# Kernel tuning notes

Hardware: AMD Instinct MI355X
Metric: run time of the kernel (lower is better)

Reference implementation:

```python
import jax, jax.numpy as jnp
import numpy as np

N = 50000
E = 800000
NFEAT, NHID, NCLASS = 128, 128, 40


def setup_inputs() -> dict:
    key = jax.random.key(0)
    ks = jax.random.split(key, 8)
    x = jax.random.normal(ks[0], (N, NFEAT), dtype=jnp.float32)
    edge_index = jax.random.randint(ks[1], (2, E), 0, N, dtype=jnp.int64)
    def glorot(k, fan_in, fan_out):
        s = jnp.sqrt(6.0 / (fan_in + fan_out)).astype(jnp.float32)
        return jax.random.uniform(k, (fan_in, fan_out), jnp.float32, -s, s)
    W1 = glorot(ks[2], NFEAT, NHID); b1 = jnp.zeros((NHID,), jnp.float32)
    W2 = glorot(ks[3], NHID, NHID);  b2 = jnp.zeros((NHID,), jnp.float32)
    W3 = glorot(ks[4], NHID, NCLASS); b3 = jnp.zeros((NCLASS,), jnp.float32)
    return {"x": x, "edge_index": edge_index,
            "W1": W1, "b1": b1, "W2": W2, "b2": b2, "W3": W3, "b3": b3}


def _gcn_norm(edge_index, num_nodes, dtype):
    # Add self-loops, then symmetric normalization D^-1/2 (A+I) D^-1/2 (PyG gcn_norm).
    loop = jnp.arange(num_nodes, dtype=edge_index.dtype)
    src = jnp.concatenate([edge_index[0], loop])
    dst = jnp.concatenate([edge_index[1], loop])
    deg = jax.ops.segment_sum(jnp.ones_like(src, dtype=dtype), dst, num_segments=num_nodes)
    dinv = jnp.where(deg > 0, deg ** -0.5, 0.0).astype(dtype)
    norm = dinv[src] * dinv[dst]  # [E+N]
    return src, dst, norm


def _gcn_conv(h, src, dst, norm, W, b, num_nodes):
    h = h @ W                              # dense transform first (out_dim small)
    msg = h[src] * norm[:, None]           # gather + per-edge scale
    out = jax.ops.segment_sum(msg, dst, num_segments=num_nodes)  # scatter-add
    return out + b


def reference(x, edge_index, W1, b1, W2, b2, W3, b3):
    src, dst, norm = _gcn_norm(edge_index, N, x.dtype)
    h = jax.nn.relu(_gcn_conv(x, src, dst, norm, W1, b1, N))  # dropout: eval mode (identity)
    h = jax.nn.relu(_gcn_conv(h, src, dst, norm, W2, b2, N))
    h = _gcn_conv(h, src, dst, norm, W3, b3, N)
    return jax.nn.log_softmax(h, axis=-1)
```

## Files before the change

### kernel.cpp

```cpp
#include <hip/hip_runtime.h>
#include <stdint.h>

#define NN 50000
#define NE 800000
#define GG 782
#define NB 196
#define EB 3125

typedef __attribute__((ext_vector_type(8))) short bfx8;
typedef __attribute__((ext_vector_type(4))) float f32x4;

__device__ inline unsigned short f2bf(float f) {
    union { float f; uint32_t u; } x; x.f = f;
    uint32_t u = x.u;
    return (unsigned short)((u + 0x7fffu + ((u >> 16) & 1u)) >> 16);
}
__device__ inline uint32_t pack2bf(float lo, float hi) {
    return (uint32_t)f2bf(lo) | ((uint32_t)f2bf(hi) << 16);
}
__device__ inline float bf2f(unsigned short h) {
    union { uint32_t u; float f; } c; c.u = ((uint32_t)h) << 16;
    return c.f;
}
__device__ inline float2 bfp2f2(uint32_t v) {
    union { uint32_t u; float f; } a, b;
    a.u = (v & 0xffffu) << 16;
    b.u = v & 0xffff0000u;
    return make_float2(a.f, b.f);
}
__device__ inline bfx8 ld8(const unsigned short* p) {
    union { uint4 u; bfx8 v; } c;
    c.u = *(const uint4*)p;
    return c.v;
}
__device__ inline bfx8 cvt8(float4 u, float4 v) {
    union { unsigned short s[8]; bfx8 r; } c;
    c.s[0] = f2bf(u.x); c.s[1] = f2bf(u.y); c.s[2] = f2bf(u.z); c.s[3] = f2bf(u.w);
    c.s[4] = f2bf(v.x); c.s[5] = f2bf(v.y); c.s[6] = f2bf(v.z); c.s[7] = f2bf(v.w);
    return c.r;
}

__global__ void prep(const float* __restrict__ W1, const float* __restrict__ W2,
                     const float* __restrict__ W3,
                     unsigned short* __restrict__ WT1, unsigned short* __restrict__ WT2,
                     unsigned short* __restrict__ WT3, int* __restrict__ hist) {
    int bid = blockIdx.x;
    if (bid < 152) {
        int w = bid * 256 + threadIdx.x;
        if (w < 16384) {
            int nn = w >> 7, k = w & 127;
            WT1[nn * 128 + k] = f2bf(W1[k * 128 + nn]);
        } else if (w < 32768) {
            int w2 = w - 16384, nn = w2 >> 7, k = w2 & 127;
            WT2[nn * 128 + k] = f2bf(W2[k * 128 + nn]);
        } else if (w < 38912) {
            int w2 = w - 32768, nn = w2 >> 7, k = w2 & 127;
            WT3[nn * 128 + k] = (nn < 40) ? f2bf(W3[k * 40 + nn]) : (unsigned short)0;
        }
    } else {
        int i = (bid - 152) * 256 + threadIdx.x;
        if (i < NN) hist[i] = 0;
    }
}

__global__ __launch_bounds__(256) void gemm1_hist(const float* __restrict__ X,
                                                  const unsigned short* __restrict__ WT,
                                                  unsigned short* __restrict__ G, int n,
                                                  const int* __restrict__ dst,
                                                  int* __restrict__ hist,
                                                  unsigned short* __restrict__ rank, int e) {
    if (blockIdx.x >= GG) {
        int i = (blockIdx.x - GG) * 256 + threadIdx.x;
        if (i < e) rank[i] = (unsigned short)atomicAdd(hist + dst[i], 1);
        return;
    }
    int wave = threadIdx.x >> 6;
    int lane = threadIdx.x & 63;
    int quad = lane >> 4;
    int c = lane & 15;
    int rowbase = blockIdx.x * 64 + wave * 16;

    int arow = rowbase + c;
    if (arow >= n) arow = n - 1;
    const float* ap = X + (size_t)arow * 128 + quad * 8;
    bfx8 a[4];
#pragma unroll
    for (int kc = 0; kc < 4; kc++) {
        float4 u = *(const float4*)(ap + kc * 32);
        float4 v = *(const float4*)(ap + kc * 32 + 4);
        a[kc] = cvt8(u, v);
    }

    f32x4 acc[8];
#pragma unroll
    for (int ct = 0; ct < 8; ct++) acc[ct] = (f32x4){0.f, 0.f, 0.f, 0.f};
#pragma unroll
    for (int ct = 0; ct < 8; ct++) {
        const unsigned short* bp = WT + (size_t)(ct * 16 + c) * 128 + quad * 8;
#pragma unroll
        for (int kc = 0; kc < 4; kc++) {
            bfx8 b = ld8(bp + kc * 32);
            acc[ct] = __builtin_amdgcn_mfma_f32_16x16x32_bf16(a[kc], b, acc[ct], 0, 0, 0);
        }
    }

    int r0 = rowbase + quad * 4;
    bool odd = lane & 1;
#pragma unroll
    for (int ct = 0; ct < 8; ct++) {
        float x0 = acc[ct][0], x1 = acc[ct][1], x2 = acc[ct][2], x3 = acc[ct][3];
        float y0 = __shfl_xor(x0, 1, 64), y1 = __shfl_xor(x1, 1, 64);
        float y2 = __shfl_xor(x2, 1, 64), y3 = __shfl_xor(x3, 1, 64);
        int colp = ct * 16 + (c & ~1);
        if (!odd) {
            if (r0 + 0 < n) *(uint32_t*)(&G[(size_t)(r0 + 0) * 128 + colp]) = pack2bf(x0, y0);
            if (r0 + 1 < n) *(uint32_t*)(&G[(size_t)(r0 + 1) * 128 + colp]) = pack2bf(x1, y1);
        } else {
            if (r0 + 2 < n) *(uint32_t*)(&G[(size_t)(r0 + 2) * 128 + colp]) = pack2bf(y2, x2);
            if (r0 + 3 < n) *(uint32_t*)(&G[(size_t)(r0 + 3) * 128 + colp]) = pack2bf(y3, x3);
        }
    }
}

__global__ void scan_dinv(const int* __restrict__ hist, int* row_ptr, int* bsum,
                          float* dinv, int n) {
    __shared__ int s[256];
    int tid = threadIdx.x;
    int i = blockIdx.x * 256 + tid;
    int v = (i < n) ? hist[i] : 0;
    s[tid] = v;
    __syncthreads();
#pragma unroll
    for (int off = 1; off < 256; off <<= 1) {
        int y = (tid >= off) ? s[tid - off] : 0;
        __syncthreads();
        s[tid] += y;
        __syncthreads();
    }
    if (i < n) {
        row_ptr[i] = s[tid] - v;
        dinv[i] = rsqrtf(1.0f + (float)v);
    }
    if (tid == 255) bsum[blockIdx.x] = s[255];
}

__global__ void bucket_k(const int* __restrict__ src, const int* __restrict__ dst,
                         const int* __restrict__ row_ptr, const int* __restrict__ bsum,
                         const unsigned short* __restrict__ rank,
                         unsigned short* __restrict__ csr_src, int* __restrict__ boff_g,
                         int e) {
    __shared__ int s[256];
    __shared__ int bex[256];
    int tid = threadIdx.x;
    int v = (tid < NB) ? bsum[tid] : 0;
    s[tid] = v;
    __syncthreads();
#pragma unroll
    for (int off = 1; off < 256; off <<= 1) {
        int y = (tid >= off) ? s[tid - off] : 0;
        __syncthreads();
        s[tid] += y;
        __syncthreads();
    }
    bex[tid] = s[tid] - v;
    __syncthreads();

    if (blockIdx.x == gridDim.x - 1) {
        if (tid < NB) boff_g[tid] = bex[tid];
        return;
    }
    int i = blockIdx.x * 256 + tid;
    if (i < e) {
        int d = dst[i];
        csr_src[row_ptr[d] + bex[d >> 8] + (int)rank[i]] = (unsigned short)src[i];
    }
}

__global__ __launch_bounds__(256) void gemm128_mfma(const unsigned short* __restrict__ A,
                                                    const unsigned short* __restrict__ WT,
                                                    const float* __restrict__ dinv,
                                                    unsigned short* __restrict__ G, int n) {
    int wave = threadIdx.x >> 6;
    int lane = threadIdx.x & 63;
    int quad = lane >> 4;
    int c = lane & 15;
    int rowbase = blockIdx.x * 64 + wave * 16;

    int arow = rowbase + c;
    if (arow >= n) arow = n - 1;
    const unsigned short* ap = A + (size_t)arow * 128 + quad * 8;
    bfx8 a[4];
#pragma unroll
    for (int kc = 0; kc < 4; kc++) a[kc] = ld8(ap + kc * 32);

    f32x4 acc[8];
#pragma unroll
    for (int ct = 0; ct < 8; ct++) acc[ct] = (f32x4){0.f, 0.f, 0.f, 0.f};
#pragma unroll
    for (int ct = 0; ct < 8; ct++) {
        const unsigned short* bp = WT + (size_t)(ct * 16 + c) * 128 + quad * 8;
#pragma unroll
        for (int kc = 0; kc < 4; kc++) {
            bfx8 b = ld8(bp + kc * 32);
            acc[ct] = __builtin_amdgcn_mfma_f32_16x16x32_bf16(a[kc], b, acc[ct], 0, 0, 0);
        }
    }

    int r0 = rowbase + quad * 4;
    float di[4];
#pragma unroll
    for (int r = 0; r < 4; r++) {
        int rr = r0 + r;
        di[r] = dinv[rr < n ? rr : 0];
    }
    bool odd = lane & 1;
#pragma unroll
    for (int ct = 0; ct < 8; ct++) {
        float x0 = acc[ct][0], x1 = acc[ct][1], x2 = acc[ct][2], x3 = acc[ct][3];
        float y0 = __shfl_xor(x0, 1, 64), y1 = __shfl_xor(x1, 1, 64);
        float y2 = __shfl_xor(x2, 1, 64), y3 = __shfl_xor(x3, 1, 64);
        int colp = ct * 16 + (c & ~1);
        if (!odd) {
            if (r0 + 0 < n) *(uint32_t*)(&G[(size_t)(r0 + 0) * 128 + colp]) = pack2bf(di[0] * x0, di[0] * y0);
            if (r0 + 1 < n) *(uint32_t*)(&G[(size_t)(r0 + 1) * 128 + colp]) = pack2bf(di[1] * x1, di[1] * y1);
        } else {
            if (r0 + 2 < n) *(uint32_t*)(&G[(size_t)(r0 + 2) * 128 + colp]) = pack2bf(di[2] * y2, di[2] * x2);
            if (r0 + 3 < n) *(uint32_t*)(&G[(size_t)(r0 + 3) * 128 + colp]) = pack2bf(di[3] * y3, di[3] * x3);
        }
    }
}

__global__ __launch_bounds__(256) void gemm40_mfma(const unsigned short* __restrict__ A,
                                                   const unsigned short* __restrict__ WT,
                                                   const float* __restrict__ dinv,
                                                   unsigned short* __restrict__ G, int n) {
    int wave = threadIdx.x >> 6;
    int lane = threadIdx.x & 63;
    int quad = lane >> 4;
    int c = lane & 15;
    int rowbase = blockIdx.x * 64 + wave * 16;

    int arow = rowbase + c;
    if (arow >= n) arow = n - 1;
    const unsigned short* ap = A + (size_t)arow * 128 + quad * 8;
    bfx8 a[4];
#pragma unroll
    for (int kc = 0; kc < 4; kc++) a[kc] = ld8(ap + kc * 32);

    f32x4 acc[3];
#pragma unroll
    for (int ct = 0; ct < 3; ct++) acc[ct] = (f32x4){0.f, 0.f, 0.f, 0.f};
#pragma unroll
    for (int ct = 0; ct < 3; ct++) {
        const unsigned short* bp = WT + (size_t)(ct * 16 + c) * 128 + quad * 8;
#pragma unroll
        for (int kc = 0; kc < 4; kc++) {
            bfx8 b = ld8(bp + kc * 32);
            acc[ct] = __builtin_amdgcn_mfma_f32_16x16x32_bf16(a[kc], b, acc[ct], 0, 0, 0);
        }
    }

    int r0 = rowbase + quad * 4;
    float di[4];
#pragma unroll
    for (int r = 0; r < 4; r++) {
        int rr = r0 + r;
        di[r] = dinv[rr < n ? rr : 0];
    }
    bool odd = lane & 1;
#pragma unroll
    for (int ct = 0; ct < 3; ct++) {
        float x0 = acc[ct][0], x1 = acc[ct][1], x2 = acc[ct][2], x3 = acc[ct][3];
        float y0 = __shfl_xor(x0, 1, 64), y1 = __shfl_xor(x1, 1, 64);
        float y2 = __shfl_xor(x2, 1, 64), y3 = __shfl_xor(x3, 1, 64);
        int colp = ct * 16 + (c & ~1);
        if (colp >= 40) continue;
        if (!odd) {
            if (r0 + 0 < n) *(uint32_t*)(&G[(size_t)(r0 + 0) * 40 + colp]) = pack2bf(di[0] * x0, di[0] * y0);
            if (r0 + 1 < n) *(uint32_t*)(&G[(size_t)(r0 + 1) * 40 + colp]) = pack2bf(di[1] * x1, di[1] * y1);
        } else {
            if (r0 + 2 < n) *(uint32_t*)(&G[(size_t)(r0 + 2) * 40 + colp]) = pack2bf(di[2] * y2, di[2] * x2);
            if (r0 + 3 < n) *(uint32_t*)(&G[(size_t)(r0 + 3) * 40 + colp]) = pack2bf(di[3] * y3, di[3] * x3);
        }
    }
}

__global__ __launch_bounds__(256) void agg128_l1(const unsigned short* __restrict__ G,
                                                 const int* __restrict__ row_ptr,
                                                 const int* __restrict__ boff,
                                                 const int* __restrict__ hist,
                                                 const unsigned short* __restrict__ csr_src,
                                                 const float* __restrict__ dinv,
                                                 const float* __restrict__ b,
                                                 unsigned short* __restrict__ Y, int n) {
    int node = blockIdx.x * 4 + (threadIdx.x >> 6);
    if (node >= n) return;
    int l = threadIdx.x & 63;
    const uint32_t* Gr = (const uint32_t*)G;

    float dn = dinv[node];
    float2 sf = bfp2f2(Gr[(size_t)node * 64 + l]);
    float2 acc = make_float2(dn * sf.x, dn * sf.y);
    int p = row_ptr[node] + boff[node >> 8];
    int p1 = p + hist[node];
    for (; p + 7 < p1; p += 8) {
        int s0 = csr_src[p],     s1 = csr_src[p + 1], s2 = csr_src[p + 2], s3 = csr_src[p + 3];
        int s4 = csr_src[p + 4], s5 = csr_src[p + 5], s6 = csr_src[p + 6], s7 = csr_src[p + 7];
        float d0 = dinv[s0], d1 = dinv[s1], d2 = dinv[s2], d3 = dinv[s3];
        float d4 = dinv[s4], d5 = dinv[s5], d6 = dinv[s6], d7 = dinv[s7];
        float2 f0 = bfp2f2(Gr[(size_t)s0 * 64 + l]), f1 = bfp2f2(Gr[(size_t)s1 * 64 + l]);
        float2 f2 = bfp2f2(Gr[(size_t)s2 * 64 + l]), f3 = bfp2f2(Gr[(size_t)s3 * 64 + l]);
        float2 f4 = bfp2f2(Gr[(size_t)s4 * 64 + l]), f5 = bfp2f2(Gr[(size_t)s5 * 64 + l]);
        float2 f6 = bfp2f2(Gr[(size_t)s6 * 64 + l]), f7 = bfp2f2(Gr[(size_t)s7 * 64 + l]);
        acc.x += (fmaf(d0, f0.x, d1 * f1.x) + fmaf(d2, f2.x, d3 * f3.x)) +
                 (fmaf(d4, f4.x, d5 * f5.x) + fmaf(d6, f6.x, d7 * f7.x));
        acc.y += (fmaf(d0, f0.y, d1 * f1.y) + fmaf(d2, f2.y, d3 * f3.y)) +
                 (fmaf(d4, f4.y, d5 * f5.y) + fmaf(d6, f6.y, d7 * f7.y));
    }
    for (; p < p1; ++p) {
        int s = csr_src[p];
        float ds = dinv[s];
        float2 f = bfp2f2(Gr[(size_t)s * 64 + l]);
        acc.x = fmaf(ds, f.x, acc.x);
        acc.y = fmaf(ds, f.y, acc.y);
    }
    float vx = fmaf(dn, acc.x, b[2 * l]);
    float vy = fmaf(dn, acc.y, b[2 * l + 1]);
    ((uint32_t*)Y)[(size_t)node * 64 + l] = pack2bf(vx > 0.f ? vx : 0.f, vy > 0.f ? vy : 0.f);
}

__global__ __launch_bounds__(256) void agg128(const unsigned short* __restrict__ G,
                                              const int* __restrict__ row_ptr,
                                              const int* __restrict__ boff,
                                              const int* __restrict__ hist,
                                              const unsigned short* __restrict__ csr_src,
                                              const float* __restrict__ dinv,
                                              const float* __restrict__ b,
                                              unsigned short* __restrict__ Y, int n) {
    int node = blockIdx.x * 4 + (threadIdx.x >> 6);
    if (node >= n) return;
    int l = threadIdx.x & 63;
    const uint32_t* Gr = (const uint32_t*)G;

    float2 acc = bfp2f2(Gr[(size_t)node * 64 + l]);
    int p = row_ptr[node] + boff[node >> 8];
    int p1 = p + hist[node];
    for (; p + 7 < p1; p += 8) {
        int s0 = csr_src[p],     s1 = csr_src[p + 1], s2 = csr_src[p + 2], s3 = csr_src[p + 3];
        int s4 = csr_src[p + 4], s5 = csr_src[p + 5], s6 = csr_src[p + 6], s7 = csr_src[p + 7];
        float2 f0 = bfp2f2(Gr[(size_t)s0 * 64 + l]), f1 = bfp2f2(Gr[(size_t)s1 * 64 + l]);
        float2 f2 = bfp2f2(Gr[(size_t)s2 * 64 + l]), f3 = bfp2f2(Gr[(size_t)s3 * 64 + l]);
        float2 f4 = bfp2f2(Gr[(size_t)s4 * 64 + l]), f5 = bfp2f2(Gr[(size_t)s5 * 64 + l]);
        float2 f6 = bfp2f2(Gr[(size_t)s6 * 64 + l]), f7 = bfp2f2(Gr[(size_t)s7 * 64 + l]);
        acc.x += ((f0.x + f1.x) + (f2.x + f3.x)) + ((f4.x + f5.x) + (f6.x + f7.x));
        acc.y += ((f0.y + f1.y) + (f2.y + f3.y)) + ((f4.y + f5.y) + (f6.y + f7.y));
    }
    for (; p < p1; ++p) {
        float2 f = bfp2f2(Gr[(size_t)csr_src[p] * 64 + l]);
        acc.x += f.x; acc.y += f.y;
    }
    float dn = dinv[node];
    float vx = fmaf(dn, acc.x, b[2 * l]);
    float vy = fmaf(dn, acc.y, b[2 * l + 1]);
    ((uint32_t*)Y)[(size_t)node * 64 + l] = pack2bf(vx > 0.f ? vx : 0.f, vy > 0.f ? vy : 0.f);
}

__global__ __launch_bounds__(256) void agg40_lsm(const unsigned short* __restrict__ G,
                                                 const int* __restrict__ row_ptr,
                                                 const int* __restrict__ boff,
                                                 const int* __restrict__ hist,
                                                 const unsigned short* __restrict__ csr_src,
                                                 const float* __restrict__ dinv,
                                                 const float* __restrict__ b,
                                                 float* __restrict__ Y, int n) {
    int node = blockIdx.x * 4 + (threadIdx.x >> 6);
    if (node >= n) return;
    int lane = threadIdx.x & 63;
    bool act = lane < 40;
    int lc = act ? lane : 0;

    float acc = act ? bf2f(G[(size_t)node * 40 + lane]) : 0.f;
    int p = row_ptr[node] + boff[node >> 8];
    int p1 = p + hist[node];
    for (; p + 3 < p1; p += 4) {
        int s0 = csr_src[p], s1 = csr_src[p + 1], s2 = csr_src[p + 2], s3 = csr_src[p + 3];
        float f0 = bf2f(G[(size_t)s0 * 40 + lc]);
        float f1 = bf2f(G[(size_t)s1 * 40 + lc]);
        float f2 = bf2f(G[(size_t)s2 * 40 + lc]);
        float f3 = bf2f(G[(size_t)s3 * 40 + lc]);
        acc += (f0 + f1) + (f2 + f3);
    }
    for (; p < p1; ++p) acc += bf2f(G[(size_t)csr_src[p] * 40 + lc]);

    float v = act ? fmaf(dinv[node], acc, b[lane]) : -1e30f;
    float m = v;
#pragma unroll
    for (int off = 32; off > 0; off >>= 1) m = fmaxf(m, __shfl_xor(m, off, 64));
    float ex = act ? expf(v - m) : 0.f;
    float s_ = ex;
#pragma unroll
    for (int off = 32; off > 0; off >>= 1) s_ += __shfl_xor(s_, off, 64);
    float ls = logf(s_);
    if (act) Y[(size_t)node * 40 + lane] = v - m - ls;
}


extern "C" void kernel_launch(void* const* d_in, const int* in_sizes, int n_in,
                              void* d_out, int out_size, void* d_ws, size_t ws_size,
                              hipStream_t stream) {
    const float* x  = (const float*)d_in[0];
    const int*   ei = (const int*)d_in[1];
    const float* W1 = (const float*)d_in[2];
    const float* b1 = (const float*)d_in[3];
    const float* W2 = (const float*)d_in[4];
    const float* b2 = (const float*)d_in[5];
    const float* W3 = (const float*)d_in[6];
    const float* b3 = (const float*)d_in[7];
    float* out = (float*)d_out;

    const int n = NN, e = NE;
    const int* srcI = ei;
    const int* dstI = ei + e;

    char* ws = (char*)d_ws;
    int*            hist    = (int*)ws;
    int*            row_ptr = (int*)(ws + 200704);
    int*            bsum    = (int*)(ws + 401408);
    int*            boff    = (int*)(ws + 402432);
    float*          dinv    = (float*)(ws + 403456);
    unsigned short* rank    = (unsigned short*)(ws + 604160);
    unsigned short* csr_src = (unsigned short*)(ws + 2204160);
    unsigned short* WT1     = (unsigned short*)(ws + 3804160);
    unsigned short* WT2     = (unsigned short*)(ws + 3836928);
    unsigned short* WT3     = (unsigned short*)(ws + 3869696);
    unsigned short* bufG    = (unsigned short*)(ws + 3881984);
    unsigned short* bufA    = (unsigned short*)(ws + 16681984);

    prep<<<152 + NB, 256, 0, stream>>>(W1, W2, W3, WT1, WT2, WT3, hist);
    gemm1_hist<<<GG + EB, 256, 0, stream>>>(x, WT1, bufG, n, dstI, hist, rank, e);
    scan_dinv<<<NB, 256, 0, stream>>>(hist, row_ptr, bsum, dinv, n);
    bucket_k<<<EB + 1, 256, 0, stream>>>(srcI, dstI, row_ptr, bsum, rank, csr_src, boff, e);
    agg128_l1<<<(n + 3) / 4, 256, 0, stream>>>(bufG, row_ptr, boff, hist, csr_src, dinv, b1, bufA, n);
    gemm128_mfma<<<GG, 256, 0, stream>>>(bufA, WT2, dinv, bufG, n);
    agg128<<<(n + 3) / 4, 256, 0, stream>>>(bufG, row_ptr, boff, hist, csr_src, dinv, b2, bufA, n);
    gemm40_mfma<<<GG, 256, 0, stream>>>(bufA, WT3, dinv, bufG, n);
    agg40_lsm<<<(n + 3) / 4, 256, 0, stream>>>(bufG, row_ptr, boff, hist, csr_src, dinv, b3, out, n);
}
```

Measured before the change: 296.0 us.

## Fuse neighbor aggregation with following MFMA GEMM through LDS staging

Merges each 128-wide aggregation kernel with the next layer's MFMA GEMM. Each wave aggregates 16 nodes one after another into a padded LDS tile, then reads its A fragments from LDS instead of global memory. This removes the write and re-read of the intermediate activation buffer and two kernel launches. The cost is far fewer waves in flight during the latency-bound gather (782 blocks instead of 12500, with each wave working through 16 nodes serially), so hiding memory latency may suffer.

```diff
diff --git a/kernel.cpp b/kernel.cpp
--- a/kernel.cpp
+++ b/kernel.cpp
@@ -6,6 +6,7 @@
 #define GG 782
 #define NB 196
 #define EB 3125
+#define LDSROW 136
 
 typedef __attribute__((ext_vector_type(8))) short bfx8;
 typedef __attribute__((ext_vector_type(4))) float f32x4;
@@ -29,6 +30,11 @@
     return make_float2(a.f, b.f);
 }
 __device__ inline bfx8 ld8(const unsigned short* p) {
+    union { uint4 u; bfx8 v; } c;
+    c.u = *(const uint4*)p;
+    return c.v;
+}
+__device__ inline bfx8 ld8_lds(const unsigned short* p) {
     union { uint4 u; bfx8 v; } c;
     c.u = *(const uint4*)p;
     return c.v;
@@ -176,22 +182,64 @@
     }
 }
 
-__global__ __launch_bounds__(256) void gemm128_mfma(const unsigned short* __restrict__ A,
-                                                    const unsigned short* __restrict__ WT,
-                                                    const float* __restrict__ dinv,
-                                                    unsigned short* __restrict__ G, int n) {
+__global__ __launch_bounds__(256) void agg1_gemm2(const unsigned short* __restrict__ G,
+                                                  const int* __restrict__ row_ptr,
+                                                  const int* __restrict__ boff,
+                                                  const int* __restrict__ hist,
+                                                  const unsigned short* __restrict__ csr_src,
+                                                  const float* __restrict__ dinv,
+                                                  const float* __restrict__ b,
+                                                  const unsigned short* __restrict__ WT,
+                                                  unsigned short* __restrict__ Gout, int n) {
+    __shared__ unsigned short As[4 * 16 * LDSROW];
     int wave = threadIdx.x >> 6;
     int lane = threadIdx.x & 63;
+    int rowbase = blockIdx.x * 64 + wave * 16;
+    unsigned short* myA = As + wave * 16 * LDSROW;
+    const uint32_t* Gr = (const uint32_t*)G;
+    int l = lane;
+
+    for (int i = 0; i < 16; i++) {
+        int node = rowbase + i;
+        uint32_t* wp = (uint32_t*)(myA + i * LDSROW);
+        if (node >= n) { wp[l] = 0; continue; }
+        float dn = dinv[node];
+        float2 sf = bfp2f2(Gr[(size_t)node * 64 + l]);
+        float2 acc = make_float2(dn * sf.x, dn * sf.y);
+        int p = row_ptr[node] + boff[node >> 8];
+        int p1 = p + hist[node];
+        for (; p + 7 < p1; p += 8) {
+            int s0 = csr_src[p],     s1 = csr_src[p + 1], s2 = csr_src[p + 2], s3 = csr_src[p + 3];
+            int s4 = csr_src[p + 4], s5 = csr_src[p + 5], s6 = csr_src[p + 6], s7 = csr_src[p + 7];
+            float d0 = dinv[s0], d1 = dinv[s1], d2 = dinv[s2], d3 = dinv[s3];
+            float d4 = dinv[s4], d5 = dinv[s5], d6 = dinv[s6], d7 = dinv[s7];
+            float2 f0 = bfp2f2(Gr[(size_t)s0 * 64 + l]), f1 = bfp2f2(Gr[(size_t)s1 * 64 + l]);
+            float2 f2 = bfp2f2(Gr[(size_t)s2 * 64 + l]), f3 = bfp2f2(Gr[(size_t)s3 * 64 + l]);
+            float2 f4 = bfp2f2(Gr[(size_t)s4 * 64 + l]), f5 = bfp2f2(Gr[(size_t)s5 * 64 + l]);
+            float2 f6 = bfp2f2(Gr[(size_t)s6 * 64 + l]), f7 = bfp2f2(Gr[(size_t)s7 * 64 + l]);
+            acc.x += (fmaf(d0, f0.x, d1 * f1.x) + fmaf(d2, f2.x, d3 * f3.x)) +
+                     (fmaf(d4, f4.x, d5 * f5.x) + fmaf(d6, f6.x, d7 * f7.x));
+            acc.y += (fmaf(d0, f0.y, d1 * f1.y) + fmaf(d2, f2.y, d3 * f3.y)) +
+                     (fmaf(d4, f4.y, d5 * f5.y) + fmaf(d6, f6.y, d7 * f7.y));
+        }
+        for (; p < p1; ++p) {
+            int s = csr_src[p];
+            float ds = dinv[s];
+            float2 f = bfp2f2(Gr[(size_t)s * 64 + l]);
+            acc.x = fmaf(ds, f.x, acc.x);
+            acc.y = fmaf(ds, f.y, acc.y);
+        }
+        float vx = fmaf(dn, acc.x, b[2 * l]);
+        float vy = fmaf(dn, acc.y, b[2 * l + 1]);
+        wp[l] = pack2bf(vx > 0.f ? vx : 0.f, vy > 0.f ? vy : 0.f);
+    }
+
     int quad = lane >> 4;
     int c = lane & 15;
-    int rowbase = blockIdx.x * 64 + wave * 16;
-
-    int arow = rowbase + c;
-    if (arow >= n) arow = n - 1;
-    const unsigned short* ap = A + (size_t)arow * 128 + quad * 8;
     bfx8 a[4];
 #pragma unroll
-    for (int kc = 0; kc < 4; kc++) a[kc] = ld8(ap + kc * 32);
+    for (int kc = 0; kc < 4; kc++)
+        a[kc] = ld8_lds(myA + c * LDSROW + quad * 8 + kc * 32);
 
     f32x4 acc[8];
 #pragma unroll
@@ -201,8 +249,8 @@
         const unsigned short* bp = WT + (size_t)(ct * 16 + c) * 128 + quad * 8;
 #pragma unroll
         for (int kc = 0; kc < 4; kc++) {
-            bfx8 b = ld8(bp + kc * 32);
-            acc[ct] = __builtin_amdgcn_mfma_f32_16x16x32_bf16(a[kc], b, acc[ct], 0, 0, 0);
+            bfx8 bb = ld8(bp + kc * 32);
+            acc[ct] = __builtin_amdgcn_mfma_f32_16x16x32_bf16(a[kc], bb, acc[ct], 0, 0, 0);
         }
     }
 
@@ -221,31 +269,65 @@
         float y2 = __shfl_xor(x2, 1, 64), y3 = __shfl_xor(x3, 1, 64);
         int colp = ct * 16 + (c & ~1);
         if (!odd) {
-            if (r0 + 0 < n) *(uint32_t*)(&G[(size_t)(r0 + 0) * 128 + colp]) = pack2bf(di[0] * x0, di[0] * y0);
-            if (r0 + 1 < n) *(uint32_t*)(&G[(size_t)(r0 + 1) * 128 + colp]) = pack2bf(di[1] * x1, di[1] * y1);
+            if (r0 + 0 < n) *(uint32_t*)(&Gout[(size_t)(r0 + 0) * 128 + colp]) = pack2bf(di[0] * x0, di[0] * y0);
+            if (r0 + 1 < n) *(uint32_t*)(&Gout[(size_t)(r0 + 1) * 128 + colp]) = pack2bf(di[1] * x1, di[1] * y1);
         } else {
-            if (r0 + 2 < n) *(uint32_t*)(&G[(size_t)(r0 + 2) * 128 + colp]) = pack2bf(di[2] * y2, di[2] * x2);
-            if (r0 + 3 < n) *(uint32_t*)(&G[(size_t)(r0 + 3) * 128 + colp]) = pack2bf(di[3] * y3, di[3] * x3);
-        }
-    }
-}
-
-__global__ __launch_bounds__(256) void gemm40_mfma(const unsigned short* __restrict__ A,
-                                                   const unsigned short* __restrict__ WT,
-                                                   const float* __restrict__ dinv,
-                                                   unsigned short* __restrict__ G, int n) {
+            if (r0 + 2 < n) *(uint32_t*)(&Gout[(size_t)(r0 + 2) * 128 + colp]) = pack2bf(di[2] * y2, di[2] * x2);
+            if (r0 + 3 < n) *(uint32_t*)(&Gout[(size_t)(r0 + 3) * 128 + colp]) = pack2bf(di[3] * y3, di[3] * x3);
+        }
+    }
+}
+
+__global__ __launch_bounds__(256) void agg2_gemm3(const unsigned short* __restrict__ G,
+                                                  const int* __restrict__ row_ptr,
+                                                  const int* __restrict__ boff,
+                                                  const int* __restrict__ hist,
+                                                  const unsigned short* __restrict__ csr_src,
+                                                  const float* __restrict__ dinv,
+                                                  const float* __restrict__ b,
+                                                  const unsigned short* __restrict__ WT,
+                                                  unsigned short* __restrict__ Gout, int n) {
+    __shared__ unsigned short As[4 * 16 * LDSROW];
     int wave = threadIdx.x >> 6;
     int lane = threadIdx.x & 63;
+    int rowbase = blockIdx.x * 64 + wave * 16;
+    unsigned short* myA = As + wave * 16 * LDSROW;
+    const uint32_t* Gr = (const uint32_t*)G;
+    int l = lane;
+
+    for (int i = 0; i < 16; i++) {
+        int node = rowbase + i;
+        uint32_t* wp = (uint32_t*)(myA + i * LDSROW);
+        if (node >= n) { wp[l] = 0; continue; }
+        float2 acc = bfp2f2(Gr[(size_t)node * 64 + l]);
+        int p = row_ptr[node] + boff[node >> 8];
+        int p1 = p + hist[node];
+        for (; p + 7 < p1; p += 8) {
+            int s0 = csr_src[p],     s1 = csr_src[p + 1], s2 = csr_src[p + 2], s3 = csr_src[p + 3];
+            int s4 = csr_src[p + 4], s5 = csr_src[p + 5], s6 = csr_src[p + 6], s7 = csr_src[p + 7];
+            float2 f0 = bfp2f2(Gr[(size_t)s0 * 64 + l]), f1 = bfp2f2(Gr[(size_t)s1 * 64 + l]);
+            float2 f2 = bfp2f2(Gr[(size_t)s2 * 64 + l]), f3 = bfp2f2(Gr[(size_t)s3 * 64 + l]);
+            float2 f4 = bfp2f2(Gr[(size_t)s4 * 64 + l]), f5 = bfp2f2(Gr[(size_t)s5 * 64 + l]);
+            float2 f6 = bfp2f2(Gr[(size_t)s6 * 64 + l]), f7 = bfp2f2(Gr[(size_t)s7 * 64 + l]);
+            acc.x += ((f0.x + f1.x) + (f2.x + f3.x)) + ((f4.x + f5.x) + (f6.x + f7.x));
+            acc.y += ((f0.y + f1.y) + (f2.y + f3.y)) + ((f4.y + f5.y) + (f6.y + f7.y));
+        }
+        for (; p < p1; ++p) {
+            float2 f = bfp2f2(Gr[(size_t)csr_src[p] * 64 + l]);
+            acc.x += f.x; acc.y += f.y;
+        }
+        float dn = dinv[node];
+        float vx = fmaf(dn, acc.x, b[2 * l]);
+        float vy = fmaf(dn, acc.y, b[2 * l + 1]);
+        wp[l] = pack2bf(vx > 0.f ? vx : 0.f, vy > 0.f ? vy : 0.f);
+    }
+
     int quad = lane >> 4;
     int c = lane & 15;
-    int rowbase = blockIdx.x * 64 + wave * 16;
-
-    int arow = rowbase + c;
-    if (arow >= n) arow = n - 1;
-    const unsigned short* ap = A + (size_t)arow * 128 + quad * 8;
     bfx8 a[4];
 #pragma unroll
-    for (int kc = 0; kc < 4; kc++) a[kc] = ld8(ap + kc * 32);
+    for (int kc = 0; kc < 4; kc++)
+        a[kc] = ld8_lds(myA + c * LDSROW + quad * 8 + kc * 32);
 
     f32x4 acc[3];
 #pragma unroll
@@ -255,8 +337,8 @@
         const unsigned short* bp = WT + (size_t)(ct * 16 + c) * 128 + quad * 8;
 #pragma unroll
         for (int kc = 0; kc < 4; kc++) {
-            bfx8 b = ld8(bp + kc * 32);
-            acc[ct] = __builtin_amdgcn_mfma_f32_16x16x32_bf16(a[kc], b, acc[ct], 0, 0, 0);
+            bfx8 bb = ld8(bp + kc * 32);
+            acc[ct] = __builtin_amdgcn_mfma_f32_16x16x32_bf16(a[kc], bb, acc[ct], 0, 0, 0);
         }
     }
 
@@ -276,93 +358,13 @@
         int colp = ct * 16 + (c & ~1);
         if (colp >= 40) continue;
         if (!odd) {
-            if (r0 + 0 < n) *(uint32_t*)(&G[(size_t)(r0 + 0) * 40 + colp]) = pack2bf(di[0] * x0, di[0] * y0);
-            if (r0 + 1 < n) *(uint32_t*)(&G[(size_t)(r0 + 1) * 40 + colp]) = pack2bf(di[1] * x1, di[1] * y1);
+            if (r0 + 0 < n) *(uint32_t*)(&Gout[(size_t)(r0 + 0) * 40 + colp]) = pack2bf(di[0] * x0, di[0] * y0);
+            if (r0 + 1 < n) *(uint32_t*)(&Gout[(size_t)(r0 + 1) * 40 + colp]) = pack2bf(di[1] * x1, di[1] * y1);
         } else {
-            if (r0 + 2 < n) *(uint32_t*)(&G[(size_t)(r0 + 2) * 40 + colp]) = pack2bf(di[2] * y2, di[2] * x2);
-            if (r0 + 3 < n) *(uint32_t*)(&G[(size_t)(r0 + 3) * 40 + colp]) = pack2bf(di[3] * y3, di[3] * x3);
-        }
-    }
-}
-
-__global__ __launch_bounds__(256) void agg128_l1(const unsigned short* __restrict__ G,
-                                                 const int* __restrict__ row_ptr,
-                                                 const int* __restrict__ boff,
-                                                 const int* __restrict__ hist,
-                                                 const unsigned short* __restrict__ csr_src,
-                                                 const float* __restrict__ dinv,
-                                                 const float* __restrict__ b,
-                                                 unsigned short* __restrict__ Y, int n) {
-    int node = blockIdx.x * 4 + (threadIdx.x >> 6);
-    if (node >= n) return;
-    int l = threadIdx.x & 63;
-    const uint32_t* Gr = (const uint32_t*)G;
-
-    float dn = dinv[node];
-    float2 sf = bfp2f2(Gr[(size_t)node * 64 + l]);
-    float2 acc = make_float2(dn * sf.x, dn * sf.y);
-    int p = row_ptr[node] + boff[node >> 8];
-    int p1 = p + hist[node];
-    for (; p + 7 < p1; p += 8) {
-        int s0 = csr_src[p],     s1 = csr_src[p + 1], s2 = csr_src[p + 2], s3 = csr_src[p + 3];
-        int s4 = csr_src[p + 4], s5 = csr_src[p + 5], s6 = csr_src[p + 6], s7 = csr_src[p + 7];
-        float d0 = dinv[s0], d1 = dinv[s1], d2 = dinv[s2], d3 = dinv[s3];
-        float d4 = dinv[s4], d5 = dinv[s5], d6 = dinv[s6], d7 = dinv[s7];
-        float2 f0 = bfp2f2(Gr[(size_t)s0 * 64 + l]), f1 = bfp2f2(Gr[(size_t)s1 * 64 + l]);
-        float2 f2 = bfp2f2(Gr[(size_t)s2 * 64 + l]), f3 = bfp2f2(Gr[(size_t)s3 * 64 + l]);
-        float2 f4 = bfp2f2(Gr[(size_t)s4 * 64 + l]), f5 = bfp2f2(Gr[(size_t)s5 * 64 + l]);
-        float2 f6 = bfp2f2(Gr[(size_t)s6 * 64 + l]), f7 = bfp2f2(Gr[(size_t)s7 * 64 + l]);
-        acc.x += (fmaf(d0, f0.x, d1 * f1.x) + fmaf(d2, f2.x, d3 * f3.x)) +
-                 (fmaf(d4, f4.x, d5 * f5.x) + fmaf(d6, f6.x, d7 * f7.x));
-        acc.y += (fmaf(d0, f0.y, d1 * f1.y) + fmaf(d2, f2.y, d3 * f3.y)) +
-                 (fmaf(d4, f4.y, d5 * f5.y) + fmaf(d6, f6.y, d7 * f7.y));
-    }
-    for (; p < p1; ++p) {
-        int s = csr_src[p];
-        float ds = dinv[s];
-        float2 f = bfp2f2(Gr[(size_t)s * 64 + l]);
-        acc.x = fmaf(ds, f.x, acc.x);
-        acc.y = fmaf(ds, f.y, acc.y);
-    }
-    float vx = fmaf(dn, acc.x, b[2 * l]);
-    float vy = fmaf(dn, acc.y, b[2 * l + 1]);
-    ((uint32_t*)Y)[(size_t)node * 64 + l] = pack2bf(vx > 0.f ? vx : 0.f, vy > 0.f ? vy : 0.f);
-}
-
-__global__ __launch_bounds__(256) void agg128(const unsigned short* __restrict__ G,
-                                              const int* __restrict__ row_ptr,
-                                              const int* __restrict__ boff,
-                                              const int* __restrict__ hist,
-                                              const unsigned short* __restrict__ csr_src,
-                                              const float* __restrict__ dinv,
-                                              const float* __restrict__ b,
-                                              unsigned short* __restrict__ Y, int n) {
-    int node = blockIdx.x * 4 + (threadIdx.x >> 6);
-    if (node >= n) return;
-    int l = threadIdx.x & 63;
-    const uint32_t* Gr = (const uint32_t*)G;
-
-    float2 acc = bfp2f2(Gr[(size_t)node * 64 + l]);
-    int p = row_ptr[node] + boff[node >> 8];
-    int p1 = p + hist[node];
-    for (; p + 7 < p1; p += 8) {
-        int s0 = csr_src[p],     s1 = csr_src[p + 1], s2 = csr_src[p + 2], s3 = csr_src[p + 3];
-        int s4 = csr_src[p + 4], s5 = csr_src[p + 5], s6 = csr_src[p + 6], s7 = csr_src[p + 7];
-        float2 f0 = bfp2f2(Gr[(size_t)s0 * 64 + l]), f1 = bfp2f2(Gr[(size_t)s1 * 64 + l]);
-        float2 f2 = bfp2f2(Gr[(size_t)s2 * 64 + l]), f3 = bfp2f2(Gr[(size_t)s3 * 64 + l]);
-        float2 f4 = bfp2f2(Gr[(size_t)s4 * 64 + l]), f5 = bfp2f2(Gr[(size_t)s5 * 64 + l]);
-        float2 f6 = bfp2f2(Gr[(size_t)s6 * 64 + l]), f7 = bfp2f2(Gr[(size_t)s7 * 64 + l]);
-        acc.x += ((f0.x + f1.x) + (f2.x + f3.x)) + ((f4.x + f5.x) + (f6.x + f7.x));
-        acc.y += ((f0.y + f1.y) + (f2.y + f3.y)) + ((f4.y + f5.y) + (f6.y + f7.y));
-    }
-    for (; p < p1; ++p) {
-        float2 f = bfp2f2(Gr[(size_t)csr_src[p] * 64 + l]);
-        acc.x += f.x; acc.y += f.y;
-    }
-    float dn = dinv[node];
-    float vx = fmaf(dn, acc.x, b[2 * l]);
-    float vy = fmaf(dn, acc.y, b[2 * l + 1]);
-    ((uint32_t*)Y)[(size_t)node * 64 + l] = pack2bf(vx > 0.f ? vx : 0.f, vy > 0.f ? vy : 0.f);
+            if (r0 + 2 < n) *(uint32_t*)(&Gout[(size_t)(r0 + 2) * 40 + colp]) = pack2bf(di[2] * y2, di[2] * x2);
+            if (r0 + 3 < n) *(uint32_t*)(&Gout[(size_t)(r0 + 3) * 40 + colp]) = pack2bf(di[3] * y3, di[3] * x3);
+        }
+    }
 }
 
 __global__ __launch_bounds__(256) void agg40_lsm(const unsigned short* __restrict__ G,
@@ -434,15 +436,14 @@
     unsigned short* WT2     = (unsigned short*)(ws + 3836928);
     unsigned short* WT3     = (unsigned short*)(ws + 3869696);
     unsigned short* bufG    = (unsigned short*)(ws + 3881984);
-    unsigned short* bufA    = (unsigned short*)(ws + 16681984);
+    unsigned short* bufB    = (unsigned short*)(ws + 16681984);
+    unsigned short* G40     = bufG;
 
     prep<<<152 + NB, 256, 0, stream>>>(W1, W2, W3, WT1, WT2, WT3, hist);
     gemm1_hist<<<GG + EB, 256, 0, stream>>>(x, WT1, bufG, n, dstI, hist, rank, e);
     scan_dinv<<<NB, 256, 0, stream>>>(hist, row_ptr, bsum, dinv, n);
     bucket_k<<<EB + 1, 256, 0, stream>>>(srcI, dstI, row_ptr, bsum, rank, csr_src, boff, e);
-    agg128_l1<<<(n + 3) / 4, 256, 0, stream>>>(bufG, row_ptr, boff, hist, csr_src, dinv, b1, bufA, n);
-    gemm128_mfma<<<GG, 256, 0, stream>>>(bufA, WT2, dinv, bufG, n);
-    agg128<<<(n + 3) / 4, 256, 0, stream>>>(bufG, row_ptr, boff, hist, csr_src, dinv, b2, bufA, n);
-    gemm40_mfma<<<GG, 256, 0, stream>>>(bufA, WT3, dinv, bufG, n);
-    agg40_lsm<<<(n + 3) / 4, 256, 0, stream>>>(bufG, row_ptr, boff, hist, csr_src, dinv, b3, out, n);
-}
+    agg1_gemm2<<<GG, 256, 0, stream>>>(bufG, row_ptr, boff, hist, csr_src, dinv, b1, WT2, bufB, n);
+    agg2_gemm3<<<GG, 256, 0, stream>>>(bufB, row_ptr, boff, hist, csr_src, dinv, b2, WT3, G40, n);
+    agg40_lsm<<<(n + 3) / 4, 256, 0, stream>>>(G40, row_ptr, boff, hist, csr_src, dinv, b3, out, n);
+}
```

Result: slower. 335.3 us (+13.3%).
